# Kernel optimization log

Hardware: AMD Instinct MI355X
Metric: run time of the kernel (lower is better)

## Reference

```python
import jax, jax.numpy as jnp
import numpy as np

K = 3; STRIDE = 1; PAD = 1; DIL = 1; KN = K * K * K  # num_pts = 27


def _trilinear_sample(vol, grid):
    """F.grid_sample 3D, mode=bilinear, padding=zeros, align_corners=False.
    vol: (C, D, H, W); grid: (od, oh, ow, 3) with xyz order in [-1, 1].
    Returns (C, od, oh, ow)."""
    C, D, H, W = vol.shape
    # unnormalize (align_corners=False)
    ix = ((grid[..., 0] + 1.0) * W - 1.0) * 0.5
    iy = ((grid[..., 1] + 1.0) * H - 1.0) * 0.5
    iz = ((grid[..., 2] + 1.0) * D - 1.0) * 0.5
    x0 = jnp.floor(ix); y0 = jnp.floor(iy); z0 = jnp.floor(iz)
    out = jnp.zeros((C,) + grid.shape[:-1], vol.dtype)
    for dz in (0, 1):
        for dy in (0, 1):
            for dx in (0, 1):
                xc = x0 + dx; yc = y0 + dy; zc = z0 + dz
                w = (1.0 - jnp.abs(ix - xc)) * (1.0 - jnp.abs(iy - yc)) * (1.0 - jnp.abs(iz - zc))
                valid = (xc >= 0) & (xc < W) & (yc >= 0) & (yc < H) & (zc >= 0) & (zc < D)
                xi = jnp.clip(xc, 0, W - 1).astype(jnp.int32)
                yi = jnp.clip(yc, 0, H - 1).astype(jnp.int32)
                zi = jnp.clip(zc, 0, D - 1).astype(jnp.int32)
                val = vol[:, zi, yi, xi]  # (C, od, oh, ow)
                out = out + val * (w * valid.astype(vol.dtype))[None]
    return out


def setup_inputs() -> dict:
    key = jax.random.key(0)
    k1, k2, k3 = jax.random.split(key, 3)
    N, C, D, H, W = 2, 64, 16, 32, 32
    inp = jax.random.normal(k1, (N, C, D, H, W), dtype=jnp.float32)
    offset = jax.random.normal(k2, (N, KN * 3, D, H, W), dtype=jnp.float32)
    weight = jax.random.normal(k3, (64, 64, KN), dtype=jnp.float32) * 0.05
    return {"input": inp, "offset": offset, "weight": weight}


def reference(input, offset, weight):
    N, C, D, H, W = input.shape
    od, oh, ow = offset.shape[2], offset.shape[3], offset.shape[4]
    f32 = input.dtype
    # base sampling mesh (align_corners=True style normalization, as original)
    z = (jnp.arange(od) * STRIDE - PAD + ((K - 1) // 2) * DIL).astype(f32)
    y = (jnp.arange(oh) * STRIDE - PAD + ((K - 1) // 2) * DIL).astype(f32)
    x = (jnp.arange(ow) * STRIDE - PAD + ((K - 1) // 2) * DIL).astype(f32)
    mz, my, mx = jnp.meshgrid(z, y, x, indexing="ij")
    norm = lambda v, S: (v - (S - 1) / 2.0) / ((S - 1) / 2.0)
    mesh = jnp.stack([norm(mx, W), norm(my, H), norm(mz, D)], axis=-1)  # (od,oh,ow,3)
    # offsets: channel layout per kernel point is (dz, dy, dx)
    off = offset.reshape(N, KN, 3, od, oh, ow)
    goff = jnp.stack([
        off[:, :, 2] / ((W - 1) / 2.0),
        off[:, :, 1] / ((H - 1) / 2.0),
        off[:, :, 0] / ((D - 1) / 2.0),
    ], axis=-1)  # (N, KN, od, oh, ow, 3) xyz
    grid = mesh[None, None] + goff
    # per-batch, per-kernel-point trilinear gather -> (N, KN, C, od, oh, ow)
    sampled = jax.vmap(lambda v, g: jax.vmap(lambda gg: _trilinear_sample(v, gg))(g))(input, grid)
    # grouped matmul: weight (O, C, KN) flattened C-major matches sampled layout
    out = jnp.einsum("ock,nkcdhw->nodhw", weight, sampled)
    return out
```

## Files before the change

### kernel.cpp

```cpp
#include <hip/hip_runtime.h>

typedef __attribute__((ext_vector_type(8))) _Float16 half8;
typedef __attribute__((ext_vector_type(4))) float floatx4;

constexpr int NB  = 2;
constexpr int CC  = 64;
constexpr int DD  = 16;
constexpr int HH  = 32;
constexpr int WW  = 32;
constexpr int KN_ = 27;
constexpr int OC  = 64;
constexpr int DHW = DD * HH * WW;
constexpr int TP  = 32;

__device__ __forceinline__ unsigned short f2h(float f) {
    _Float16 h = (_Float16)f;
    return *(unsigned short*)&h;
}

__global__ __launch_bounds__(256) void k_prep(const float* __restrict__ in,
                                              const float* __restrict__ w,
                                              unsigned int* __restrict__ outu,
                                              unsigned short* __restrict__ wf) {
    int bid = blockIdx.x;
    int t = threadIdx.x;
    if (bid < 512) {
        __shared__ float tile[64][65];
        int n  = bid >> 8;
        int v0 = (bid & 255) << 6;
        int lane = t & 63, row = t >> 6;
#pragma unroll
        for (int i = 0; i < 16; ++i) {
            int c = (i << 2) + row;
            tile[c][lane] = in[(size_t)(n * CC + c) * DHW + v0 + lane];
        }
        __syncthreads();
#pragma unroll
        for (int i = 0; i < 8; ++i) {
            int flat = i * 256 + t;
            int v = flat >> 5, cd = flat & 31;
            unsigned int lo = f2h(tile[2 * cd][v]);
            unsigned int hi = f2h(tile[2 * cd + 1][v]);
            outu[(size_t)(n * DHW + v0 + v) * 32 + cd] = lo | (hi << 16);
        }
    } else {
        int f = (bid - 512) * 256 + t;
        int i  = f & 7;
        int l  = (f >> 3) & 63;
        int ot = (f >> 9) & 3;
        int cc = (f >> 11) & 1;
        int k  = f >> 12;
        int o = ot * 16 + (l & 15);
        int c = cc * 32 + ((l >> 4) << 3) + i;
        wf[f] = f2h(w[(o * CC + c) * KN_ + k]);
    }
}

__global__ __launch_bounds__(256, 4) void k_main(const unsigned short* __restrict__ inp,
                                                 const unsigned short* __restrict__ wf,
                                                 const float* __restrict__ offs,
                                                 float* __restrict__ out) {
    __shared__ unsigned short S[2 * TP * 64];
    __shared__ uint4 SUV[KN_ * TP];
    __shared__ uint4 SUW[KN_ * TP];

    int t   = threadIdx.x;
    int bid = blockIdx.x;
    int n   = (bid >> 2) & 1;
    int idx = ((bid >> 3) << 2) | (bid & 3);
    int p0  = idx << 5;

    int sp = t >> 3;
    int cg = t & 7;
    int w  = t >> 6;
    int l  = t & 63;
    int lrow = l & 15, lk = l >> 4;

    const float* offb = offs + (size_t)n * (3 * KN_) * DHW + p0;
    const char*  inb  = (const char*)(inp + ((size_t)n * DHW << 6));

    floatx4 acc0 = {0.f, 0.f, 0.f, 0.f};
    floatx4 acc1 = {0.f, 0.f, 0.f, 0.f};

    const int cgo  = cg << 4;
    const int woff = sp * 64 + ((cg ^ (sp & 7)) << 3);
    const int r0   = lrow;
    const int r1   = 16 + lrow;
    const int roff00 = r0 * 64 + (((0 | lk) ^ (r0 & 7)) << 3);
    const int roff01 = r0 * 64 + (((4 | lk) ^ (r0 & 7)) << 3);
    const int roff10 = r1 * 64 + (((0 | lk) ^ (r1 & 7)) << 3);
    const int roff11 = r1 * 64 + (((4 | lk) ^ (r1 & 7)) << 3);

    for (int si = t; si < KN_ * TP; si += 256) {
        int k = si >> 5, p = si & 31;
        int pa = p0 + p;
        int dpos = pa >> 10, hpos = (pa >> 5) & 31, wpos = pa & 31;

        float oz = offb[(k * 3 + 0) * DHW + p];
        float oy = offb[(k * 3 + 1) * DHW + p];
        float ox = offb[(k * 3 + 2) * DHW + p];
        float ix = ((float)wpos + ox) * (32.0f / 31.0f) - 0.5f;
        float iy = ((float)hpos + oy) * (32.0f / 31.0f) - 0.5f;
        float iz = ((float)dpos + oz) * (16.0f / 15.0f) - 0.5f;
        float xf = floorf(ix), yf = floorf(iy), zf = floorf(iz);
        float fx = ix - xf, fy = iy - yf, fz = iz - zf;
        int x0 = (int)xf, y0 = (int)yf, z0 = (int)zf;

        float wx0 = ((unsigned)x0       < (unsigned)WW) ? 1.f - fx : 0.f;
        float wx1 = ((unsigned)(x0 + 1) < (unsigned)WW) ? fx       : 0.f;
        float wy0 = ((unsigned)y0       < (unsigned)HH) ? 1.f - fy : 0.f;
        float wy1 = ((unsigned)(y0 + 1) < (unsigned)HH) ? fy       : 0.f;
        float wz0 = ((unsigned)z0       < (unsigned)DD) ? 1.f - fz : 0.f;
        float wz1 = ((unsigned)(z0 + 1) < (unsigned)DD) ? fz       : 0.f;

        int xc0 = min(max(x0, 0), WW - 1), xc1 = min(max(x0 + 1, 0), WW - 1);
        int yc0 = min(max(y0, 0), HH - 1), yc1 = min(max(y0 + 1, 0), HH - 1);
        int zc0 = min(max(z0, 0), DD - 1), zc1 = min(max(z0 + 1, 0), DD - 1);

        float wzy00 = wz0 * wy0, wzy01 = wz0 * wy1, wzy10 = wz1 * wy0, wzy11 = wz1 * wy1;
        unsigned int b00 = (zc0 * HH + yc0) * WW, b01 = (zc0 * HH + yc1) * WW;
        unsigned int b10 = (zc1 * HH + yc0) * WW, b11 = (zc1 * HH + yc1) * WW;

        uint4 vp, wp;
        vp.x = (b00 + xc0) | ((b00 + xc1) << 16);
        vp.y = (b01 + xc0) | ((b01 + xc1) << 16);
        vp.z = (b10 + xc0) | ((b10 + xc1) << 16);
        vp.w = (b11 + xc0) | ((b11 + xc1) << 16);
        wp.x = (unsigned int)f2h(wzy00 * wx0) | ((unsigned int)f2h(wzy00 * wx1) << 16);
        wp.y = (unsigned int)f2h(wzy01 * wx0) | ((unsigned int)f2h(wzy01 * wx1) << 16);
        wp.z = (unsigned int)f2h(wzy10 * wx0) | ((unsigned int)f2h(wzy10 * wx1) << 16);
        wp.w = (unsigned int)f2h(wzy11 * wx0) | ((unsigned int)f2h(wzy11 * wx1) << 16);

        SUV[si] = vp;
        SUW[si] = wp;
    }
    __syncthreads();

    for (int k = 0; k < KN_; ++k) {
        const half8 wa0 = *(const half8*)(wf + (((((k << 1) | 0) << 2) + w) << 9) + (l << 3));
        const half8 wa1 = *(const half8*)(wf + (((((k << 1) | 1) << 2) + w) << 9) + (l << 3));

        const uint4 vp = SUV[(k << 5) + sp];
        const uint4 wp = SUW[(k << 5) + sp];
        const unsigned int vpa[4] = {vp.x, vp.y, vp.z, vp.w};
        const unsigned int wpa[4] = {wp.x, wp.y, wp.z, wp.w};

        half8 accv = {0, 0, 0, 0, 0, 0, 0, 0};
#pragma unroll
        for (int cr = 0; cr < 8; ++cr) {
            unsigned int vd = vpa[cr >> 1];
            unsigned int voxb = ((cr & 1) ? (vd >> 16) : (vd & 0xffffu)) << 7;
            unsigned int wd = wpa[cr >> 1];
            unsigned short wu = (cr & 1) ? (unsigned short)(wd >> 16) : (unsigned short)wd;
            _Float16 wh = *(_Float16*)&wu;
            const half8 v = *(const half8*)(inb + voxb + cgo);
            half8 w8 = {wh, wh, wh, wh, wh, wh, wh, wh};
            accv += v * w8;
        }
        *(half8*)(S + ((k & 1) << 11) + woff) = accv;

        __syncthreads();

        const unsigned short* Sb = S + ((k & 1) << 11);
        const half8 bf00 = *(const half8*)(Sb + roff00);
        const half8 bf01 = *(const half8*)(Sb + roff01);
        const half8 bf10 = *(const half8*)(Sb + roff10);
        const half8 bf11 = *(const half8*)(Sb + roff11);
        acc0 = __builtin_amdgcn_mfma_f32_16x16x32_f16(wa0, bf00, acc0, 0, 0, 0);
        acc0 = __builtin_amdgcn_mfma_f32_16x16x32_f16(wa1, bf01, acc0, 0, 0, 0);
        acc1 = __builtin_amdgcn_mfma_f32_16x16x32_f16(wa0, bf10, acc1, 0, 0, 0);
        acc1 = __builtin_amdgcn_mfma_f32_16x16x32_f16(wa1, bf11, acc1, 0, 0, 0);
    }

    float* ob = out + ((size_t)n * OC + (w << 4) + (lk << 2)) * DHW + p0 + lrow;
#pragma unroll
    for (int r = 0; r < 4; ++r) {
        ob[r * DHW]      = acc0[r];
        ob[r * DHW + 16] = acc1[r];
    }
}

__global__ __launch_bounds__(256) void k_fallback(const float* __restrict__ inp,
                                                  const float* __restrict__ wt,
                                                  const float* __restrict__ offs,
                                                  float* __restrict__ out) {
    __shared__ float Slds[64][68];
    __shared__ float Wlds[64 * 64];
    int bid = blockIdx.x;
    int n = bid >> 8;
    int p0 = (bid & 255) * 64;
    int t = threadIdx.x;
    int cq = t & 15, c0 = cq << 2, pslot = t >> 4;
    int ob = (t & 15) << 2, pb = (t >> 4) << 2;
    int swz_w = (((cq & 7) ^ (cq >> 3)) << 2);
    float acc[4][4] = {};
    const float* offbase = offs + (size_t)n * (KN_ * 3) * DHW;
    for (int k = 0; k < KN_; ++k) {
#pragma unroll
        for (int i = 0; i < 16; ++i) {
            int f = i * 256 + t;
            int o = f & 63, c = f >> 6;
            Wlds[f] = wt[(o * CC + c) * KN_ + k];
        }
#pragma unroll
        for (int j = 0; j < 4; ++j) {
            int pl = pslot + 16 * j;
            int pa = p0 + pl;
            int d = pa >> 10, h = (pa >> 5) & 31, w = pa & 31;
            float offz = offbase[(k * 3 + 0) * DHW + pa];
            float offy = offbase[(k * 3 + 1) * DHW + pa];
            float offx = offbase[(k * 3 + 2) * DHW + pa];
            float ix = ((float)w + offx) * (32.0f / 31.0f) - 0.5f;
            float iy = ((float)h + offy) * (32.0f / 31.0f) - 0.5f;
            float iz = ((float)d + offz) * (16.0f / 15.0f) - 0.5f;
            float xf = floorf(ix), yf = floorf(iy), zf = floorf(iz);
            float fx = ix - xf, fy = iy - yf, fz = iz - zf;
            int x0 = (int)xf, y0 = (int)yf, z0 = (int)zf;
            float wx0 = 1.0f - fx, wx1 = fx, wy0 = 1.0f - fy, wy1 = fy, wz0 = 1.0f - fz, wz1 = fz;
            float s0 = 0.f, s1 = 0.f, s2 = 0.f, s3 = 0.f;
#pragma unroll
            for (int dz = 0; dz < 2; ++dz) {
                int zc = z0 + dz;
                if ((unsigned)zc >= (unsigned)DD) continue;
                float wz = dz ? wz1 : wz0;
#pragma unroll
                for (int dy = 0; dy < 2; ++dy) {
                    int yc = y0 + dy;
                    if ((unsigned)yc >= (unsigned)HH) continue;
                    float wzy = wz * (dy ? wy1 : wy0);
#pragma unroll
                    for (int dx = 0; dx < 2; ++dx) {
                        int xc = x0 + dx;
                        if ((unsigned)xc >= (unsigned)WW) continue;
                        float wf = wzy * (dx ? wx1 : wx0);
                        int vox = (zc * HH + yc) * WW + xc;
                        const float* b = inp + (size_t)(n * CC + c0) * DHW + vox;
                        s0 += wf * b[0]; s1 += wf * b[DHW];
                        s2 += wf * b[2 * DHW]; s3 += wf * b[3 * DHW];
                    }
                }
            }
            int plw = pl ^ swz_w;
            Slds[c0 + 0][plw] = s0; Slds[c0 + 1][plw] = s1;
            Slds[c0 + 2][plw] = s2; Slds[c0 + 3][plw] = s3;
        }
        __syncthreads();
#pragma unroll
        for (int c = 0; c < 64; ++c) {
            const int g = ((c >> 2) & 7) ^ (c >> 5);
            float4 wv = *(const float4*)(Wlds + c * 64 + ob);
            float4 sv = *(const float4*)(&Slds[c][pb ^ (g << 2)]);
            float wa[4] = {wv.x, wv.y, wv.z, wv.w};
            float sa[4] = {sv.x, sv.y, sv.z, sv.w};
#pragma unroll
            for (int i = 0; i < 4; ++i)
#pragma unroll
                for (int jj = 0; jj < 4; ++jj) acc[i][jj] += wa[i] * sa[jj];
        }
        __syncthreads();
    }
#pragma unroll
    for (int i = 0; i < 4; ++i) {
        float4 vv;
        vv.x = acc[i][0]; vv.y = acc[i][1]; vv.z = acc[i][2]; vv.w = acc[i][3];
        *(float4*)(out + (size_t)(n * OC + ob + i) * DHW + p0 + pb) = vv;
    }
}

extern "C" void kernel_launch(void* const* d_in, const int* in_sizes, int n_in,
                              void* d_out, int out_size, void* d_ws, size_t ws_size,
                              hipStream_t stream) {
    const float* inp = (const float*)d_in[0];
    const float* off = (const float*)d_in[1];
    const float* wgt = (const float*)d_in[2];
    float* out = (float*)d_out;

    const size_t in_f16_bytes = (size_t)NB * DHW * CC * 2;
    const size_t wf_bytes     = (size_t)KN_ * 2 * 4 * 64 * 8 * 2;

    if (ws_size >= in_f16_bytes + wf_bytes) {
        unsigned int*   in_t = (unsigned int*)d_ws;
        unsigned short* w_f  = (unsigned short*)((char*)d_ws + in_f16_bytes);
        k_prep<<<dim3(512 + 432), dim3(256), 0, stream>>>(inp, wgt, in_t, w_f);
        k_main<<<dim3(1024), dim3(256), 0, stream>>>(
            (const unsigned short*)in_t, w_f, off, out);
    } else {
        k_fallback<<<dim3(NB * 256), dim3(256), 0, stream>>>(inp, wgt, off, out);
    }
}
```

Measured before the change: 109.7 us.

## Double point tile per block and chunk kernel-point sampling metadata

After: 131.0 us. 1.19x slower.

```diff
diff --git a/kernel.cpp b/kernel.cpp
--- a/kernel.cpp
+++ b/kernel.cpp
@@ -11,7 +11,8 @@
 constexpr int KN_ = 27;
 constexpr int OC  = 64;
 constexpr int DHW = DD * HH * WW;
-constexpr int TP  = 32;
+constexpr int TP  = 64;
+constexpr int KCH = 9;
 
 __device__ __forceinline__ unsigned short f2h(float f) {
     _Float16 h = (_Float16)f;
@@ -61,14 +62,14 @@
                                                  const float* __restrict__ offs,
                                                  float* __restrict__ out) {
     __shared__ unsigned short S[2 * TP * 64];
-    __shared__ uint4 SUV[KN_ * TP];
-    __shared__ uint4 SUW[KN_ * TP];
+    __shared__ uint4 SUV[KCH * TP];
+    __shared__ uint4 SUW[KCH * TP];
 
     int t   = threadIdx.x;
     int bid = blockIdx.x;
     int n   = (bid >> 2) & 1;
     int idx = ((bid >> 3) << 2) | (bid & 3);
-    int p0  = idx << 5;
+    int p0  = idx << 6;
 
     int sp = t >> 3;
     int cg = t & 7;
@@ -81,95 +82,114 @@
 
     floatx4 acc0 = {0.f, 0.f, 0.f, 0.f};
     floatx4 acc1 = {0.f, 0.f, 0.f, 0.f};
-
-    const int cgo  = cg << 4;
-    const int woff = sp * 64 + ((cg ^ (sp & 7)) << 3);
-    const int r0   = lrow;
-    const int r1   = 16 + lrow;
-    const int roff00 = r0 * 64 + (((0 | lk) ^ (r0 & 7)) << 3);
-    const int roff01 = r0 * 64 + (((4 | lk) ^ (r0 & 7)) << 3);
-    const int roff10 = r1 * 64 + (((0 | lk) ^ (r1 & 7)) << 3);
-    const int roff11 = r1 * 64 + (((4 | lk) ^ (r1 & 7)) << 3);
-
-    for (int si = t; si < KN_ * TP; si += 256) {
-        int k = si >> 5, p = si & 31;
-        int pa = p0 + p;
-        int dpos = pa >> 10, hpos = (pa >> 5) & 31, wpos = pa & 31;
-
-        float oz = offb[(k * 3 + 0) * DHW + p];
-        float oy = offb[(k * 3 + 1) * DHW + p];
-        float ox = offb[(k * 3 + 2) * DHW + p];
-        float ix = ((float)wpos + ox) * (32.0f / 31.0f) - 0.5f;
-        float iy = ((float)hpos + oy) * (32.0f / 31.0f) - 0.5f;
-        float iz = ((float)dpos + oz) * (16.0f / 15.0f) - 0.5f;
-        float xf = floorf(ix), yf = floorf(iy), zf = floorf(iz);
-        float fx = ix - xf, fy = iy - yf, fz = iz - zf;
-        int x0 = (int)xf, y0 = (int)yf, z0 = (int)zf;
-
-        float wx0 = ((unsigned)x0       < (unsigned)WW) ? 1.f - fx : 0.f;
-        float wx1 = ((unsigned)(x0 + 1) < (unsigned)WW) ? fx       : 0.f;
-        float wy0 = ((unsigned)y0       < (unsigned)HH) ? 1.f - fy : 0.f;
-        float wy1 = ((unsigned)(y0 + 1) < (unsigned)HH) ? fy       : 0.f;
-        float wz0 = ((unsigned)z0       < (unsigned)DD) ? 1.f - fz : 0.f;
-        float wz1 = ((unsigned)(z0 + 1) < (unsigned)DD) ? fz       : 0.f;
-
-        int xc0 = min(max(x0, 0), WW - 1), xc1 = min(max(x0 + 1, 0), WW - 1);
-        int yc0 = min(max(y0, 0), HH - 1), yc1 = min(max(y0 + 1, 0), HH - 1);
-        int zc0 = min(max(z0, 0), DD - 1), zc1 = min(max(z0 + 1, 0), DD - 1);
-
-        float wzy00 = wz0 * wy0, wzy01 = wz0 * wy1, wzy10 = wz1 * wy0, wzy11 = wz1 * wy1;
-        unsigned int b00 = (zc0 * HH + yc0) * WW, b01 = (zc0 * HH + yc1) * WW;
-        unsigned int b10 = (zc1 * HH + yc0) * WW, b11 = (zc1 * HH + yc1) * WW;
-
-        uint4 vp, wp;
-        vp.x = (b00 + xc0) | ((b00 + xc1) << 16);
-        vp.y = (b01 + xc0) | ((b01 + xc1) << 16);
-        vp.z = (b10 + xc0) | ((b10 + xc1) << 16);
-        vp.w = (b11 + xc0) | ((b11 + xc1) << 16);
-        wp.x = (unsigned int)f2h(wzy00 * wx0) | ((unsigned int)f2h(wzy00 * wx1) << 16);
-        wp.y = (unsigned int)f2h(wzy01 * wx0) | ((unsigned int)f2h(wzy01 * wx1) << 16);
-        wp.z = (unsigned int)f2h(wzy10 * wx0) | ((unsigned int)f2h(wzy10 * wx1) << 16);
-        wp.w = (unsigned int)f2h(wzy11 * wx0) | ((unsigned int)f2h(wzy11 * wx1) << 16);
-
-        SUV[si] = vp;
-        SUW[si] = wp;
-    }
-    __syncthreads();
-
-    for (int k = 0; k < KN_; ++k) {
-        const half8 wa0 = *(const half8*)(wf + (((((k << 1) | 0) << 2) + w) << 9) + (l << 3));
-        const half8 wa1 = *(const half8*)(wf + (((((k << 1) | 1) << 2) + w) << 9) + (l << 3));
-
-        const uint4 vp = SUV[(k << 5) + sp];
-        const uint4 wp = SUW[(k << 5) + sp];
-        const unsigned int vpa[4] = {vp.x, vp.y, vp.z, vp.w};
-        const unsigned int wpa[4] = {wp.x, wp.y, wp.z, wp.w};
-
-        half8 accv = {0, 0, 0, 0, 0, 0, 0, 0};
-#pragma unroll
-        for (int cr = 0; cr < 8; ++cr) {
-            unsigned int vd = vpa[cr >> 1];
-            unsigned int voxb = ((cr & 1) ? (vd >> 16) : (vd & 0xffffu)) << 7;
-            unsigned int wd = wpa[cr >> 1];
-            unsigned short wu = (cr & 1) ? (unsigned short)(wd >> 16) : (unsigned short)wd;
-            _Float16 wh = *(_Float16*)&wu;
-            const half8 v = *(const half8*)(inb + voxb + cgo);
-            half8 w8 = {wh, wh, wh, wh, wh, wh, wh, wh};
-            accv += v * w8;
-        }
-        *(half8*)(S + ((k & 1) << 11) + woff) = accv;
-
+    floatx4 acc2 = {0.f, 0.f, 0.f, 0.f};
+    floatx4 acc3 = {0.f, 0.f, 0.f, 0.f};
+
+    const int cgo   = cg << 4;
+    const int woff0 = sp * 64 + ((cg ^ (sp & 7)) << 3);
+    const int woff1 = woff0 + 32 * 64;
+    const int roffc0 = lrow * 64 + (((0 | lk) ^ (lrow & 7)) << 3);
+    const int roffc1 = lrow * 64 + (((4 | lk) ^ (lrow & 7)) << 3);
+
+    for (int ch = 0; ch < 3; ++ch) {
+        for (int si = t; si < KCH * TP; si += 256) {
+            int kk = si >> 6, p = si & 63;
+            int k  = ch * KCH + kk;
+            int pa = p0 + p;
+            int dpos = pa >> 10, hpos = (pa >> 5) & 31, wpos = pa & 31;
+
+            float oz = offb[(k * 3 + 0) * DHW + p];
+            float oy = offb[(k * 3 + 1) * DHW + p];
+            float ox = offb[(k * 3 + 2) * DHW + p];
+            float ix = ((float)wpos + ox) * (32.0f / 31.0f) - 0.5f;
+            float iy = ((float)hpos + oy) * (32.0f / 31.0f) - 0.5f;
+            float iz = ((float)dpos + oz) * (16.0f / 15.0f) - 0.5f;
+            float xf = floorf(ix), yf = floorf(iy), zf = floorf(iz);
+            float fx = ix - xf, fy = iy - yf, fz = iz - zf;
+            int x0 = (int)xf, y0 = (int)yf, z0 = (int)zf;
+
+            float wx0 = ((unsigned)x0       < (unsigned)WW) ? 1.f - fx : 0.f;
+            float wx1 = ((unsigned)(x0 + 1) < (unsigned)WW) ? fx       : 0.f;
+            float wy0 = ((unsigned)y0       < (unsigned)HH) ? 1.f - fy : 0.f;
+            float wy1 = ((unsigned)(y0 + 1) < (unsigned)HH) ? fy       : 0.f;
+            float wz0 = ((unsigned)z0       < (unsigned)DD) ? 1.f - fz : 0.f;
+            float wz1 = ((unsigned)(z0 + 1) < (unsigned)DD) ? fz       : 0.f;
+
+            int xc0 = min(max(x0, 0), WW - 1), xc1 = min(max(x0 + 1, 0), WW - 1);
+            int yc0 = min(max(y0, 0), HH - 1), yc1 = min(max(y0 + 1, 0), HH - 1);
+            int zc0 = min(max(z0, 0), DD - 1), zc1 = min(max(z0 + 1, 0), DD - 1);
+
+            float wzy00 = wz0 * wy0, wzy01 = wz0 * wy1, wzy10 = wz1 * wy0, wzy11 = wz1 * wy1;
+            unsigned int b00 = (zc0 * HH + yc0) * WW, b01 = (zc0 * HH + yc1) * WW;
+            unsigned int b10 = (zc1 * HH + yc0) * WW, b11 = (zc1 * HH + yc1) * WW;
+
+            uint4 vp, wp;
+            vp.x = (b00 + xc0) | ((b00 + xc1) << 16);
+            vp.y = (b01 + xc0) | ((b01 + xc1) << 16);
+            vp.z = (b10 + xc0) | ((b10 + xc1) << 16);
+            vp.w = (b11 + xc0) | ((b11 + xc1) << 16);
+            wp.x = (unsigned int)f2h(wzy00 * wx0) | ((unsigned int)f2h(wzy00 * wx1) << 16);
+            wp.y = (unsigned int)f2h(wzy01 * wx0) | ((unsigned int)f2h(wzy01 * wx1) << 16);
+            wp.z = (unsigned int)f2h(wzy10 * wx0) | ((unsigned int)f2h(wzy10 * wx1) << 16);
+            wp.w = (unsigned int)f2h(wzy11 * wx0) | ((unsigned int)f2h(wzy11 * wx1) << 16);
+
+            SUV[si] = vp;
+            SUW[si] = wp;
+        }
         __syncthreads();
 
-        const unsigned short* Sb = S + ((k & 1) << 11);
-        const half8 bf00 = *(const half8*)(Sb + roff00);
-        const half8 bf01 = *(const half8*)(Sb + roff01);
-        const half8 bf10 = *(const half8*)(Sb + roff10);
-        const half8 bf11 = *(const half8*)(Sb + roff11);
-        acc0 = __builtin_amdgcn_mfma_f32_16x16x32_f16(wa0, bf00, acc0, 0, 0, 0);
-        acc0 = __builtin_amdgcn_mfma_f32_16x16x32_f16(wa1, bf01, acc0, 0, 0, 0);
-        acc1 = __builtin_amdgcn_mfma_f32_16x16x32_f16(wa0, bf10, acc1, 0, 0, 0);
-        acc1 = __builtin_amdgcn_mfma_f32_16x16x32_f16(wa1, bf11, acc1, 0, 0, 0);
+        for (int kk = 0; kk < KCH; ++kk) {
+            int k = ch * KCH + kk;
+
+            const half8 wa0 = *(const half8*)(wf + (((((k << 1) | 0) << 2) + w) << 9) + (l << 3));
+            const half8 wa1 = *(const half8*)(wf + (((((k << 1) | 1) << 2) + w) << 9) + (l << 3));
+
+            const uint4 vpA = SUV[(kk << 6) + sp];
+            const uint4 wpA = SUW[(kk << 6) + sp];
+            const uint4 vpB = SUV[(kk << 6) + sp + 32];
+            const uint4 wpB = SUW[(kk << 6) + sp + 32];
+            const unsigned int vpa[4] = {vpA.x, vpA.y, vpA.z, vpA.w};
+            const unsigned int wpa[4] = {wpA.x, wpA.y, wpA.z, wpA.w};
+            const unsigned int vpb[4] = {vpB.x, vpB.y, vpB.z, vpB.w};
+            const unsigned int wpb[4] = {wpB.x, wpB.y, wpB.z, wpB.w};
+
+            half8 accA = {0, 0, 0, 0, 0, 0, 0, 0};
+            half8 accB = {0, 0, 0, 0, 0, 0, 0, 0};
+#pragma unroll
+            for (int cr = 0; cr < 8; ++cr) {
+                unsigned int vdA = vpa[cr >> 1];
+                unsigned int vdB = vpb[cr >> 1];
+                unsigned int voxA = ((cr & 1) ? (vdA >> 16) : (vdA & 0xffffu)) << 7;
+                unsigned int voxB = ((cr & 1) ? (vdB >> 16) : (vdB & 0xffffu)) << 7;
+                unsigned int wdA = wpa[cr >> 1];
+                unsigned int wdB = wpb[cr >> 1];
+                unsigned short wuA = (cr & 1) ? (unsigned short)(wdA >> 16) : (unsigned short)wdA;
+                unsigned short wuB = (cr & 1) ? (unsigned short)(wdB >> 16) : (unsigned short)wdB;
+                _Float16 whA = *(_Float16*)&wuA;
+                _Float16 whB = *(_Float16*)&wuB;
+                const half8 vA = *(const half8*)(inb + voxA + cgo);
+                const half8 vB = *(const half8*)(inb + voxB + cgo);
+                half8 w8A = {whA, whA, whA, whA, whA, whA, whA, whA};
+                half8 w8B = {whB, whB, whB, whB, whB, whB, whB, whB};
+                accA += vA * w8A;
+                accB += vB * w8B;
+            }
+            unsigned short* Sw = S + ((k & 1) << 12);
+            *(half8*)(Sw + woff0) = accA;
+            *(half8*)(Sw + woff1) = accB;
+
+            __syncthreads();
+
+            const unsigned short* Sb = S + ((k & 1) << 12);
+#pragma unroll
+            for (int pt = 0; pt < 4; ++pt) {
+                const half8 bf0 = *(const half8*)(Sb + roffc0 + pt * 1024);
+                const half8 bf1 = *(const half8*)(Sb + roffc1 + pt * 1024);
+                floatx4* ac = (pt == 0) ? &acc0 : (pt == 1) ? &acc1 : (pt == 2) ? &acc2 : &acc3;
+                *ac = __builtin_amdgcn_mfma_f32_16x16x32_f16(wa0, bf0, *ac, 0, 0, 0);
+                *ac = __builtin_amdgcn_mfma_f32_16x16x32_f16(wa1, bf1, *ac, 0, 0, 0);
+            }
+        }
     }
 
     float* ob = out + ((size_t)n * OC + (w << 4) + (lk << 2)) * DHW + p0 + lrow;
@@ -177,6 +197,8 @@
     for (int r = 0; r < 4; ++r) {
         ob[r * DHW]      = acc0[r];
         ob[r * DHW + 16] = acc1[r];
+        ob[r * DHW + 32] = acc2[r];
+        ob[r * DHW + 48] = acc3[r];
     }
 }
 
@@ -282,7 +304,7 @@
         unsigned int*   in_t = (unsigned int*)d_ws;
         unsigned short* w_f  = (unsigned short*)((char*)d_ws + in_f16_bytes);
         k_prep<<<dim3(512 + 432), dim3(256), 0, stream>>>(inp, wgt, in_t, w_f);
-        k_main<<<dim3(1024), dim3(256), 0, stream>>>(
+        k_main<<<dim3(512), dim3(256), 0, stream>>>(
             (const unsigned short*)in_t, w_f, off, out);
     } else {
         k_fallback<<<dim3(NB * 256), dim3(256), 0, stream>>>(inp, wgt, off, out);
```
